# Kernel tuning notes

Hardware: AMD Instinct MI355X
Metric: run time of the kernel (lower is better)

## Reference

```python
import jax, jax.numpy as jnp
import numpy as np

H = 200  # hidden size
I = 129  # input features (n_fft bins)


def _lstm_layer(x, w_ih, w_hh, b_ih, b_hh):
    """PyTorch-convention LSTM. x: [B,T,I]; w_ih: [4H,I]; w_hh: [4H,H].
    Gate order i, f, g, o. Returns hidden sequence [B,T,H]."""
    B, T, _ = x.shape
    Hh = w_hh.shape[1]
    # Precompute input contribution for all timesteps (one big GEMM).
    xg = jnp.einsum('bti,gi->btg', x, w_ih) + b_ih + b_hh  # [B,T,4H]
    xg = jnp.swapaxes(xg, 0, 1)  # [T,B,4H] time-major for scan

    def step(carry, xg_t):
        h, c = carry
        g = xg_t + h @ w_hh.T  # [B,4H]
        i, f, gg, o = jnp.split(g, 4, axis=-1)
        i = jax.nn.sigmoid(i)
        f = jax.nn.sigmoid(f)
        gg = jnp.tanh(gg)
        o = jax.nn.sigmoid(o)
        c = f * c + i * gg
        h = o * jnp.tanh(c)
        return (h, c), h

    h0 = jnp.zeros((B, Hh), x.dtype)
    (_, _), hs = jax.lax.scan(step, (h0, h0), xg)
    return jnp.swapaxes(hs, 0, 1)  # [B,T,H]


def setup_inputs() -> dict:
    key = jax.random.key(0)
    ks = jax.random.split(key, 16)
    B, T = 256, 600
    s1 = 1.0 / np.sqrt(H)
    u = lambda k, shape: jax.random.uniform(k, shape, jnp.float32, -s1, s1)
    return {
        'x': jax.random.normal(ks[0], (B, I, T), jnp.float32),
        'w_ih1': u(ks[1], (4 * H, I)),
        'w_hh1': u(ks[2], (4 * H, H)),
        'b_ih1': u(ks[3], (4 * H,)),
        'b_hh1': u(ks[4], (4 * H,)),
        'w_ih2': u(ks[5], (4 * H, H)),
        'w_hh2': u(ks[6], (4 * H, H)),
        'b_ih2': u(ks[7], (4 * H,)),
        'b_hh2': u(ks[8], (4 * H,)),
        'fc1_w': u(ks[9], (I, H)),
        'fc1_b': u(ks[10], (I,)),
        'fc2_w': u(ks[11], (I, I)),
        'fc2_b': u(ks[12], (I,)),
    }


def reference(x, w_ih1, w_hh1, b_ih1, b_hh1,
              w_ih2, w_hh2, b_ih2, b_hh2,
              fc1_w, fc1_b, fc2_w, fc2_b):
    lstm_in = jnp.transpose(x, (0, 2, 1))  # [B,T,129]
    h1 = _lstm_layer(lstm_in, w_ih1, w_hh1, b_ih1, b_hh1)  # [B,T,200]
    h2 = _lstm_layer(h1, w_ih2, w_hh2, b_ih2, b_hh2)       # [B,T,200]
    y = jax.nn.relu(h2 @ fc1_w.T + fc1_b)                  # [B,T,129]
    y = jax.nn.sigmoid(y @ fc2_w.T + fc2_b)                # [B,T,129]
    return jnp.transpose(y, (0, 2, 1))                     # [B,129,T]
```

## Files before the change

### kernel.cpp

```cpp
#include <hip/hip_runtime.h>

typedef unsigned short u16;
typedef short short8 __attribute__((ext_vector_type(8)));
typedef float f32x4 __attribute__((ext_vector_type(4)));
typedef unsigned short u16x4 __attribute__((ext_vector_type(4)));

#define B_  256
#define T_  600
#define TC_ 75
#define HID 200
#define G4  800
#define HSTR 232

__device__ __forceinline__ float bf2f(u16 u) {
  union { unsigned int i; float f; } v; v.i = ((unsigned int)u) << 16; return v.f;
}
__device__ __forceinline__ u16 f2bf(float f) {
  union { float f; unsigned int i; } v; v.f = f;
  unsigned int r = v.i + 0x7FFFu + ((v.i >> 16) & 1u);
  return (u16)(r >> 16);
}
__device__ __forceinline__ float sigm(float x) {
  float e = __expf(-x);
  return __builtin_amdgcn_rcpf(1.f + e);
}

#define BARRIER_LGKM() asm volatile("s_waitcnt lgkmcnt(0)\n\ts_barrier" ::: "memory")
#define BARRIER_ONLY() asm volatile("s_barrier" ::: "memory")

__global__ __launch_bounds__(256) void padperm_k(const float* __restrict__ src,
                                                 u16* __restrict__ dst,
                                                 int rows, int srows, int scols,
                                                 int dcols, int perm) {
  int idx = blockIdx.x * 256 + threadIdx.x;
  if (idx >= rows * dcols) return;
  int r = idx / dcols, c = idx - r * dcols;
  int sr = perm ? ((r & 3) * 200 + (r >> 2)) : r;
  dst[idx] = (r < srows && c < scols) ? f2bf(src[(size_t)sr * scols + c]) : (u16)0;
}

__global__ __launch_bounds__(256) void transpose_k(const float* __restrict__ x,
                                                   u16* __restrict__ xTq, int t0) {
  __shared__ u16 tile[129 * 65];
  const int b = blockIdx.y;
  const int tt0 = blockIdx.x * 64;
  const int tid = threadIdx.x;
  for (int idx = tid; idx < 129 * 64; idx += 256) {
    int i = idx >> 6, tt = idx & 63;
    int t = t0 + tt0 + tt;
    tile[i * 65 + tt] = (tt0 + tt < TC_ && t < T_)
        ? f2bf(x[((size_t)b * 129 + i) * T_ + t]) : (u16)0;
  }
  __syncthreads();
  for (int idx = tid; idx < 64 * 160; idx += 256) {
    int tt = idx / 160, i = idx - tt * 160;
    if (tt0 + tt < TC_)
      xTq[((size_t)b * TC_ + tt0 + tt) * 160 + i] = (i < 129) ? tile[i * 65 + tt] : (u16)0;
  }
}

template<int ASRC, int LDK, int NSRC, int NSTORE, int BPERM, int ACT, int OUTM, int CHUNK>
__global__ __launch_bounds__(256, 2) void gemm_k(
    const u16* __restrict__ A, const u16* __restrict__ W,
    const float* __restrict__ B1, const float* __restrict__ B2,
    void* __restrict__ outv, int ldout, int t0) {
  constexpr int NCH = LDK / 8;
  constexpr int KT = LDK / 32;
  __shared__ u16 la[128 * LDK];
  __shared__ float lbias[128];
  const int tid = threadIdx.x;
  const int mb = blockIdx.x, nb = blockIdx.y;

  for (int idx = tid; idx < 128 * NCH; idx += 256) {
    int row = idx / NCH, c = idx - row * NCH;
    int m = mb * 128 + row;
    size_t arow;
    if (CHUNK) {
      int b = m / TC_;
      int tt = m - b * TC_;
      arow = (size_t)b * T_ + t0 + tt;
    } else {
      arow = (size_t)m;
    }
    short8 v = (short8)0;
    if (8 * c + 8 <= ASRC)
      v = *(const short8*)(A + arow * ASRC + 8 * c);
    *(short8*)(la + row * LDK + 8 * c) = v;
  }
  if (tid < 128) {
    int p = nb * 128 + tid;
    float bv = 0.f;
    if (p < NSRC) {
      int orig = BPERM ? ((p & 3) * 200 + (p >> 2)) : p;
      bv = B1[orig];
      if (BPERM) bv += B2[orig];
    }
    lbias[tid] = bv;
  }
  __syncthreads();

  const int w = tid >> 6, l = tid & 63;
  const int quad = l >> 4, l15 = l & 15;
  const int mq = (w >> 1) * 64, nq = (w & 1) * 64;

  const u16* wrow[4];
#pragma unroll
  for (int nt = 0; nt < 4; ++nt) {
    int p = nb * 128 + nq + nt * 16 + l15;
    wrow[nt] = W + (size_t)((p < NSRC) ? p : 0) * LDK;
  }

  f32x4 acc[4][4];
#pragma unroll
  for (int i = 0; i < 4; ++i)
#pragma unroll
    for (int j = 0; j < 4; ++j) acc[i][j] = (f32x4)0.f;

#pragma unroll
  for (int kt = 0; kt < KT; ++kt) {
    const int k0 = kt * 32 + quad * 8;
    short8 bf[4];
#pragma unroll
    for (int nt = 0; nt < 4; ++nt) bf[nt] = *(const short8*)(wrow[nt] + k0);
    short8 af[4];
#pragma unroll
    for (int mt = 0; mt < 4; ++mt)
      af[mt] = *(const short8*)(la + (mq + mt * 16 + l15) * LDK + k0);
#pragma unroll
    for (int mt = 0; mt < 4; ++mt)
#pragma unroll
      for (int nt = 0; nt < 4; ++nt)
        acc[mt][nt] = __builtin_amdgcn_mfma_f32_16x16x32_bf16(af[mt], bf[nt],
                                                              acc[mt][nt], 0, 0, 0);
  }

#pragma unroll
  for (int mt = 0; mt < 4; ++mt) {
#pragma unroll
    for (int nt = 0; nt < 4; ++nt) {
#pragma unroll
      for (int r = 0; r < 4; ++r) {
        int rowl = mq + mt * 16 + quad * 4 + r;
        int coln = nq + nt * 16 + l15;
        int pg = nb * 128 + coln;
        if (pg < NSTORE) {
          float v = (pg < NSRC) ? (acc[mt][nt][r] + lbias[coln]) : 0.f;
          if (ACT == 1) v = fmaxf(v, 0.f);
          if (ACT == 2) v = sigm(v);
          size_t m = (size_t)mb * 128 + rowl;
          if (OUTM == 0) {
            ((u16*)outv)[m * (size_t)ldout + pg] = f2bf(v);
          } else {
            int b = (int)(m / T_);
            int t = (int)(m - (size_t)b * T_);
            ((float*)outv)[((size_t)b * 129 + pg) * T_ + t] = v;
          }
        }
      }
    }
  }
}

__device__ __forceinline__ void rec_body(const u16* __restrict__ xgq,
                                         const u16* __restrict__ whh,
                                         u16* __restrict__ hout,
                                         float* __restrict__ cst,
                                         int t0, int blk) {
  __shared__ u16 hbuf[16 * HSTR];
  __shared__ u16 w45[50 * 2 * 512];
  __shared__ u16 w6lds[50 * 128];

  const int tid = threadIdx.x;
  const int w = tid >> 6, l = tid & 63;
  const int quad = l >> 4, l15 = l & 15;
  const int b0 = blk * 16;
  const int nslots = (w < 2) ? 4 : 3;

  short8 wreg[4][4];
#pragma unroll
  for (int s = 0; s < 4; ++s) {
    int tile = w + 16 * s;
    int p = tile * 16 + l15;
    int orig = (p & 3) * 200 + (p >> 2);
    const char* wbase = (const char*)whh + (size_t)orig * 400;
#pragma unroll
    for (int kk = 0; kk < 4; ++kk) {
      short8 v = (short8)0;
      if (s < nslots)
        v = *(const short8*)(wbase + kk * 64 + quad * 16);
      wreg[s][kk] = v;
    }
    if (s < nslots) {
#pragma unroll
      for (int j = 0; j < 2; ++j) {
        short8 v = *(const short8*)(wbase + (4 + j) * 64 + quad * 16);
        *(short8*)(w45 + ((size_t)tile * 2 + j) * 512 + l15 * 32 + quad * 8) = v;
      }
      if (quad == 0) {
        short8 v6 = *(const short8*)(wbase + 384);
        *(short8*)(w6lds + tile * 128 + l15 * 8) = v6;
      }
    }
  }
  for (int i = tid; i < 16 * HSTR; i += 1024) hbuf[i] = 0;

  float c[4];
  u16 hreg[4];
#pragma unroll
  for (int s = 0; s < 4; ++s) { c[s] = 0.f; hreg[s] = 0; }
  if (t0 != 0) {
#pragma unroll
    for (int s = 0; s < 4; ++s)
      if (s < nslots) {
        int unit = (w + 16 * s) * 4 + quad;
        hreg[s] = hout[((size_t)(b0 + l15) * T_ + (t0 - 1)) * HID + unit];
        c[s] = cst[(size_t)(b0 + l15) * HID + unit];
      }
  }

  const u16* xptr = xgq + (size_t)(b0 + l15) * TC_ * G4 + w * 16 + quad * 4;
  u16x4 xv[4];
#pragma unroll
  for (int s = 0; s < 4; ++s)
    xv[s] = (s < nslots) ? *(const u16x4*)(xptr + s * 256) : (u16x4)0;

  u16* hptr = hout + ((size_t)(b0 + l15) * T_ + t0) * HID;

  __syncthreads();

  for (int t = 0; t < TC_; ++t) {
#pragma unroll
    for (int s = 0; s < 4; ++s)
      if (s < nslots)
        hbuf[l15 * HSTR + (w + 16 * s) * 4 + quad] = hreg[s];
    BARRIER_LGKM();

    if (t > 0) {
#pragma unroll
      for (int s = 0; s < 4; ++s)
        if (s < nslots)
          hptr[(size_t)(t - 1) * HID + (w + 16 * s) * 4 + quad] = hreg[s];
    }

    f32x4 acc[4];
#pragma unroll
    for (int s = 0; s < 4; ++s) acc[s] = (f32x4)0.f;
#pragma unroll
    for (int kk = 0; kk < 4; ++kk) {
      short8 hf = *(const short8*)(hbuf + l15 * HSTR + kk * 32 + quad * 8);
#pragma unroll
      for (int s = 0; s < 4; ++s)
        if (s < nslots)
          acc[s] = __builtin_amdgcn_mfma_f32_16x16x32_bf16(wreg[s][kk], hf, acc[s], 0, 0, 0);
    }
#pragma unroll
    for (int j = 0; j < 2; ++j) {
      short8 hf = *(const short8*)(hbuf + l15 * HSTR + (4 + j) * 32 + quad * 8);
#pragma unroll
      for (int s = 0; s < 4; ++s)
        if (s < nslots) {
          short8 wz = *(const short8*)(w45 + ((size_t)(w + 16 * s) * 2 + j) * 512
                                       + l15 * 32 + quad * 8);
          acc[s] = __builtin_amdgcn_mfma_f32_16x16x32_bf16(wz, hf, acc[s], 0, 0, 0);
        }
    }
    {
      short8 hf = *(const short8*)(hbuf + l15 * HSTR + 192 + quad * 8);
#pragma unroll
      for (int s = 0; s < 4; ++s)
        if (s < nslots) {
          short8 wz = (short8)0;
          if (quad == 0)
            wz = *(const short8*)(w6lds + (w + 16 * s) * 128 + l15 * 8);
          acc[s] = __builtin_amdgcn_mfma_f32_16x16x32_bf16(wz, hf, acc[s], 0, 0, 0);
        }
    }

#pragma unroll
    for (int s = 0; s < 4; ++s) {
      if (s < nslots) {
        float vi = acc[s][0] + bf2f(xv[s][0]);
        float vf = acc[s][1] + bf2f(xv[s][1]);
        float vg = acc[s][2] + bf2f(xv[s][2]);
        float vo = acc[s][3] + bf2f(xv[s][3]);
        float iv = sigm(vi);
        float fv = sigm(vf);
        float gv = 2.f * sigm(2.f * vg) - 1.f;
        float ov = sigm(vo);
        float cn = fv * c[s] + iv * gv;
        c[s] = cn;
        float th = 2.f * sigm(2.f * cn) - 1.f;
        hreg[s] = f2bf(ov * th);
      }
    }

    if (t + 1 < TC_) {
      const u16* xp = xptr + (size_t)(t + 1) * G4;
#pragma unroll
      for (int s = 0; s < 4; ++s)
        if (s < nslots) xv[s] = *(const u16x4*)(xp + s * 256);
    }
    BARRIER_ONLY();
  }

#pragma unroll
  for (int s = 0; s < 4; ++s)
    if (s < nslots) {
      int unit = (w + 16 * s) * 4 + quad;
      hptr[(size_t)(TC_ - 1) * HID + unit] = hreg[s];
      cst[(size_t)(b0 + l15) * HID + unit] = c[s];
    }
}

__global__ __launch_bounds__(1024) void recp_k(
    const u16* __restrict__ xgA, const u16* __restrict__ whhA,
    u16* __restrict__ hA, float* __restrict__ cstA, int t0A,
    const u16* __restrict__ xgB, const u16* __restrict__ whhB,
    u16* __restrict__ hB, float* __restrict__ cstB, int t0B, int nA) {
  const int bb = blockIdx.x;
  const u16* xg; const u16* whh; u16* ho; float* cs; int t0, blk;
  if (bb < nA) { xg = xgA; whh = whhA; ho = hA; cs = cstA; t0 = t0A; blk = bb; }
  else         { xg = xgB; whh = whhB; ho = hB; cs = cstB; t0 = t0B; blk = bb - nA; }
  rec_body(xg, whh, ho, cs, t0, blk);
}

extern "C" void kernel_launch(void* const* d_in, const int* in_sizes, int n_in,
                              void* d_out, int out_size, void* d_ws, size_t ws_size,
                              hipStream_t stream) {
  (void)in_sizes; (void)n_in; (void)out_size; (void)ws_size;
  const float* x     = (const float*)d_in[0];
  const float* w_ih1 = (const float*)d_in[1];
  const float* w_hh1 = (const float*)d_in[2];
  const float* b_ih1 = (const float*)d_in[3];
  const float* b_hh1 = (const float*)d_in[4];
  const float* w_ih2 = (const float*)d_in[5];
  const float* w_hh2 = (const float*)d_in[6];
  const float* b_ih2 = (const float*)d_in[7];
  const float* b_hh2 = (const float*)d_in[8];
  const float* fc1_w = (const float*)d_in[9];
  const float* fc1_b = (const float*)d_in[10];
  const float* fc2_w = (const float*)d_in[11];
  const float* fc2_b = (const float*)d_in[12];
  float* out = (float*)d_out;

  char* ws = (char*)d_ws;
  u16*   xgA   = (u16*)(ws);
  u16*   xgB   = (u16*)(ws + 30720000LL);
  u16*   h1    = (u16*)(ws + 61440000LL);
  u16*   h2    = (u16*)(ws + 122880000LL);
  u16*   xTq   = (u16*)(ws + 184320000LL);
  float* cst1  = (float*)(ws + 190464000LL);
  float* cst2  = (float*)(ws + 190668800LL);
  u16*   wp1   = (u16*)(ws + 190873600LL);
  u16*   wp2   = (u16*)(ws + 191129600LL);
  u16*   fc1p  = (u16*)(ws + 191488000LL);
  u16*   fc2p  = (u16*)(ws + 191545792LL);
  u16*   whh1c = (u16*)(ws + 191587072LL);
  u16*   whh2c = (u16*)(ws + 191907072LL);
  u16*   y1    = h1;

  padperm_k<<<(800 * 160 + 255) / 256, 256, 0, stream>>>(w_ih1, wp1, 800, 800, 129, 160, 1);
  padperm_k<<<(800 * 224 + 255) / 256, 256, 0, stream>>>(w_ih2, wp2, 800, 800, 200, 224, 1);
  padperm_k<<<(129 * 224 + 255) / 256, 256, 0, stream>>>(fc1_w, fc1p, 129, 129, 200, 224, 0);
  padperm_k<<<(129 * 160 + 255) / 256, 256, 0, stream>>>(fc2_w, fc2p, 129, 129, 129, 160, 0);
  padperm_k<<<(800 * 200 + 255) / 256, 256, 0, stream>>>(w_hh1, whh1c, 800, 800, 200, 200, 0);
  padperm_k<<<(800 * 200 + 255) / 256, 256, 0, stream>>>(w_hh2, whh2c, 800, 800, 200, 200, 0);

  transpose_k<<<dim3(2, 256), 256, 0, stream>>>(x, xTq, 0);
  gemm_k<160, 160, 800, 800, 1, 0, 0, 0>
      <<<dim3(150, 7), 256, 0, stream>>>(xTq, wp1, b_ih1, b_hh1, xgA, 800, 0);
  recp_k<<<dim3(16), 1024, 0, stream>>>(xgA, whh1c, h1, cst1, 0,
                                        xgA, whh1c, h1, cst1, 0, 16);

  for (int i = 0; i < 7; ++i) {
    const int tA = (i + 1) * TC_;
    const int tB = i * TC_;
    transpose_k<<<dim3(2, 256), 256, 0, stream>>>(x, xTq, tA);
    gemm_k<160, 160, 800, 800, 1, 0, 0, 0>
        <<<dim3(150, 7), 256, 0, stream>>>(xTq, wp1, b_ih1, b_hh1, xgA, 800, 0);
    gemm_k<200, 224, 800, 800, 1, 0, 0, 1>
        <<<dim3(150, 7), 256, 0, stream>>>(h1, wp2, b_ih2, b_hh2, xgB, 800, tB);
    recp_k<<<dim3(32), 1024, 0, stream>>>(xgA, whh1c, h1, cst1, tA,
                                          xgB, whh2c, h2, cst2, tB, 16);
  }

  gemm_k<200, 224, 800, 800, 1, 0, 0, 1>
      <<<dim3(150, 7), 256, 0, stream>>>(h1, wp2, b_ih2, b_hh2, xgB, 800, 7 * TC_);
  recp_k<<<dim3(16), 1024, 0, stream>>>(xgA, whh1c, h1, cst1, 0,
                                        xgB, whh2c, h2, cst2, 7 * TC_, 0);

  gemm_k<200, 224, 129, 144, 0, 1, 0, 0>
      <<<dim3(1200, 2), 256, 0, stream>>>(h2, fc1p, fc1_b, fc1_b, y1, 144, 0);
  gemm_k<144, 160, 129, 129, 0, 2, 1, 0>
      <<<dim3(1200, 2), 256, 0, stream>>>(y1, fc2p, fc2_b, fc2_b, out, 0, 0);
}
```

Before: 2.759 ms.

## Double-buffer recurrent hidden-state LDS to use one barrier per timestep

Replaces the single hidden-state LDS buffer with a ping-pong pair so each step reads h from one buffer and writes the new h into the other, removing one of the two per-step barriers in the recurrent loop. The global h store now happens right after computing rather than at the start of the next step. It also specializes the per-wave slot count into explicit three-plus-optional-fourth code paths, packs the LDS into one 16-byte-aligned shared array, and pins the waves-per-EU attribute to steer register allocation. The cost is a larger LDS footprint for the second h buffer.

```diff
diff --git a/kernel.cpp b/kernel.cpp
--- a/kernel.cpp
+++ b/kernel.cpp
@@ -26,7 +26,6 @@
 }
 
 #define BARRIER_LGKM() asm volatile("s_waitcnt lgkmcnt(0)\n\ts_barrier" ::: "memory")
-#define BARRIER_ONLY() asm volatile("s_barrier" ::: "memory")
 
 __global__ __launch_bounds__(256) void padperm_k(const float* __restrict__ src,
                                                  u16* __restrict__ dst,
@@ -165,163 +164,174 @@
                                          const u16* __restrict__ whh,
                                          u16* __restrict__ hout,
                                          float* __restrict__ cst,
-                                         int t0, int blk) {
-  __shared__ u16 hbuf[16 * HSTR];
-  __shared__ u16 w45[50 * 2 * 512];
-  __shared__ u16 w6lds[50 * 128];
+                                         int t0, int blk, char* smem) {
+  u16* hb  = (u16*)smem;
+  u16* w45 = (u16*)(smem + 14848);
+  u16* w6  = (u16*)(smem + 117248);
 
   const int tid = threadIdx.x;
   const int w = tid >> 6, l = tid & 63;
   const int quad = l >> 4, l15 = l & 15;
   const int b0 = blk * 16;
-  const int nslots = (w < 2) ? 4 : 3;
+  const bool four = (w < 2);
 
   short8 wreg[4][4];
 #pragma unroll
   for (int s = 0; s < 4; ++s) {
+    const bool act = (s < 3) || four;
     int tile = w + 16 * s;
     int p = tile * 16 + l15;
     int orig = (p & 3) * 200 + (p >> 2);
-    const char* wbase = (const char*)whh + (size_t)orig * 400;
-#pragma unroll
-    for (int kk = 0; kk < 4; ++kk) {
-      short8 v = (short8)0;
-      if (s < nslots)
-        v = *(const short8*)(wbase + kk * 64 + quad * 16);
-      wreg[s][kk] = v;
-    }
-    if (s < nslots) {
-#pragma unroll
-      for (int j = 0; j < 2; ++j) {
-        short8 v = *(const short8*)(wbase + (4 + j) * 64 + quad * 16);
-        *(short8*)(w45 + ((size_t)tile * 2 + j) * 512 + l15 * 32 + quad * 8) = v;
-      }
-      if (quad == 0) {
-        short8 v6 = *(const short8*)(wbase + 384);
-        *(short8*)(w6lds + tile * 128 + l15 * 8) = v6;
-      }
-    }
-  }
-  for (int i = tid; i < 16 * HSTR; i += 1024) hbuf[i] = 0;
-
-  float c[4];
-  u16 hreg[4];
+    const u16* wb = whh + (size_t)orig * HID;
+#pragma unroll
+    for (int kk = 0; kk < 4; ++kk)
+      wreg[s][kk] = act ? *(const short8*)(wb + kk * 32 + quad * 8) : (short8)0;
+    if (act) {
+#pragma unroll
+      for (int j = 0; j < 2; ++j)
+        *(short8*)(w45 + (tile * 2 + j) * 512 + l * 8) =
+            *(const short8*)(wb + (4 + j) * 32 + quad * 8);
+      if (quad == 0)
+        *(short8*)(w6 + tile * 128 + l15 * 8) = *(const short8*)(wb + 192);
+    }
+  }
+  { int bsel = tid >> 9, r = (tid >> 5) & 15, cc = tid & 31;
+    hb[bsel * (16 * HSTR) + r * HSTR + 200 + cc] = 0; }
+
+  float c[4]; u16 hreg[4];
 #pragma unroll
   for (int s = 0; s < 4; ++s) { c[s] = 0.f; hreg[s] = 0; }
+  float* cstp = cst + (size_t)(b0 + l15) * HID;
   if (t0 != 0) {
 #pragma unroll
-    for (int s = 0; s < 4; ++s)
-      if (s < nslots) {
-        int unit = (w + 16 * s) * 4 + quad;
-        hreg[s] = hout[((size_t)(b0 + l15) * T_ + (t0 - 1)) * HID + unit];
-        c[s] = cst[(size_t)(b0 + l15) * HID + unit];
-      }
+    for (int s = 0; s < 3; ++s) {
+      int unit = (w + 16 * s) * 4 + quad;
+      hreg[s] = hout[((size_t)(b0 + l15) * T_ + (t0 - 1)) * HID + unit];
+      c[s] = cstp[unit];
+    }
+    if (four) {
+      int unit = (w + 48) * 4 + quad;
+      hreg[3] = hout[((size_t)(b0 + l15) * T_ + (t0 - 1)) * HID + unit];
+      c[3] = cstp[unit];
+    }
   }
 
   const u16* xptr = xgq + (size_t)(b0 + l15) * TC_ * G4 + w * 16 + quad * 4;
   u16x4 xv[4];
 #pragma unroll
-  for (int s = 0; s < 4; ++s)
-    xv[s] = (s < nslots) ? *(const u16x4*)(xptr + s * 256) : (u16x4)0;
+  for (int s = 0; s < 3; ++s) xv[s] = *(const u16x4*)(xptr + s * 256);
+  xv[3] = four ? *(const u16x4*)(xptr + 768) : (u16x4)0;
 
   u16* hptr = hout + ((size_t)(b0 + l15) * T_ + t0) * HID;
 
+#pragma unroll
+  for (int s = 0; s < 3; ++s)
+    hb[l15 * HSTR + (w + 16 * s) * 4 + quad] = hreg[s];
+  if (four)
+    hb[l15 * HSTR + (w + 48) * 4 + quad] = hreg[3];
+
   __syncthreads();
 
   for (int t = 0; t < TC_; ++t) {
-#pragma unroll
-    for (int s = 0; s < 4; ++s)
-      if (s < nslots)
-        hbuf[l15 * HSTR + (w + 16 * s) * 4 + quad] = hreg[s];
-    BARRIER_LGKM();
-
-    if (t > 0) {
-#pragma unroll
-      for (int s = 0; s < 4; ++s)
-        if (s < nslots)
-          hptr[(size_t)(t - 1) * HID + (w + 16 * s) * 4 + quad] = hreg[s];
-    }
+    const u16* hr = hb + (t & 1) * (16 * HSTR);
+    u16* hw = hb + ((t + 1) & 1) * (16 * HSTR);
 
     f32x4 acc[4];
 #pragma unroll
     for (int s = 0; s < 4; ++s) acc[s] = (f32x4)0.f;
+
 #pragma unroll
     for (int kk = 0; kk < 4; ++kk) {
-      short8 hf = *(const short8*)(hbuf + l15 * HSTR + kk * 32 + quad * 8);
-#pragma unroll
-      for (int s = 0; s < 4; ++s)
-        if (s < nslots)
-          acc[s] = __builtin_amdgcn_mfma_f32_16x16x32_bf16(wreg[s][kk], hf, acc[s], 0, 0, 0);
+      short8 hf = *(const short8*)(hr + l15 * HSTR + kk * 32 + quad * 8);
+      acc[0] = __builtin_amdgcn_mfma_f32_16x16x32_bf16(wreg[0][kk], hf, acc[0], 0, 0, 0);
+      acc[1] = __builtin_amdgcn_mfma_f32_16x16x32_bf16(wreg[1][kk], hf, acc[1], 0, 0, 0);
+      acc[2] = __builtin_amdgcn_mfma_f32_16x16x32_bf16(wreg[2][kk], hf, acc[2], 0, 0, 0);
+      if (four)
+        acc[3] = __builtin_amdgcn_mfma_f32_16x16x32_bf16(wreg[3][kk], hf, acc[3], 0, 0, 0);
     }
 #pragma unroll
     for (int j = 0; j < 2; ++j) {
-      short8 hf = *(const short8*)(hbuf + l15 * HSTR + (4 + j) * 32 + quad * 8);
-#pragma unroll
-      for (int s = 0; s < 4; ++s)
-        if (s < nslots) {
-          short8 wz = *(const short8*)(w45 + ((size_t)(w + 16 * s) * 2 + j) * 512
-                                       + l15 * 32 + quad * 8);
-          acc[s] = __builtin_amdgcn_mfma_f32_16x16x32_bf16(wz, hf, acc[s], 0, 0, 0);
-        }
+      short8 hf = *(const short8*)(hr + l15 * HSTR + (4 + j) * 32 + quad * 8);
+#pragma unroll
+      for (int s = 0; s < 3; ++s) {
+        short8 wz = *(const short8*)(w45 + ((w + 16 * s) * 2 + j) * 512 + l * 8);
+        acc[s] = __builtin_amdgcn_mfma_f32_16x16x32_bf16(wz, hf, acc[s], 0, 0, 0);
+      }
+      if (four) {
+        short8 wz = *(const short8*)(w45 + ((w + 48) * 2 + j) * 512 + l * 8);
+        acc[3] = __builtin_amdgcn_mfma_f32_16x16x32_bf16(wz, hf, acc[3], 0, 0, 0);
+      }
     }
     {
-      short8 hf = *(const short8*)(hbuf + l15 * HSTR + 192 + quad * 8);
-#pragma unroll
-      for (int s = 0; s < 4; ++s)
-        if (s < nslots) {
-          short8 wz = (short8)0;
-          if (quad == 0)
-            wz = *(const short8*)(w6lds + (w + 16 * s) * 128 + l15 * 8);
-          acc[s] = __builtin_amdgcn_mfma_f32_16x16x32_bf16(wz, hf, acc[s], 0, 0, 0);
-        }
+      short8 hf = *(const short8*)(hr + l15 * HSTR + 192 + quad * 8);
+#pragma unroll
+      for (int s = 0; s < 3; ++s) {
+        short8 wz = (short8)0;
+        if (quad == 0)
+          wz = *(const short8*)(w6 + (w + 16 * s) * 128 + l15 * 8);
+        acc[s] = __builtin_amdgcn_mfma_f32_16x16x32_bf16(wz, hf, acc[s], 0, 0, 0);
+      }
+      if (four) {
+        short8 wz = (short8)0;
+        if (quad == 0)
+          wz = *(const short8*)(w6 + (w + 48) * 128 + l15 * 8);
+        acc[3] = __builtin_amdgcn_mfma_f32_16x16x32_bf16(wz, hf, acc[3], 0, 0, 0);
+      }
     }
 
 #pragma unroll
     for (int s = 0; s < 4; ++s) {
-      if (s < nslots) {
-        float vi = acc[s][0] + bf2f(xv[s][0]);
-        float vf = acc[s][1] + bf2f(xv[s][1]);
-        float vg = acc[s][2] + bf2f(xv[s][2]);
-        float vo = acc[s][3] + bf2f(xv[s][3]);
-        float iv = sigm(vi);
-        float fv = sigm(vf);
-        float gv = 2.f * sigm(2.f * vg) - 1.f;
-        float ov = sigm(vo);
-        float cn = fv * c[s] + iv * gv;
-        c[s] = cn;
-        float th = 2.f * sigm(2.f * cn) - 1.f;
-        hreg[s] = f2bf(ov * th);
-      }
-    }
+      if (s == 3 && !four) break;
+      float vi = acc[s][0] + bf2f(xv[s][0]);
+      float vf = acc[s][1] + bf2f(xv[s][1]);
+      float vg = acc[s][2] + bf2f(xv[s][2]);
+      float vo = acc[s][3] + bf2f(xv[s][3]);
+      float iv = sigm(vi);
+      float fv = sigm(vf);
+      float gv = 2.f * sigm(2.f * vg) - 1.f;
+      float ov = sigm(vo);
+      float cn = fv * c[s] + iv * gv;
+      c[s] = cn;
+      float th = 2.f * sigm(2.f * cn) - 1.f;
+      hreg[s] = f2bf(ov * th);
+    }
+
+#pragma unroll
+    for (int s = 0; s < 3; ++s)
+      hw[l15 * HSTR + (w + 16 * s) * 4 + quad] = hreg[s];
+    if (four)
+      hw[l15 * HSTR + (w + 48) * 4 + quad] = hreg[3];
+
+#pragma unroll
+    for (int s = 0; s < 3; ++s)
+      hptr[(size_t)t * HID + (w + 16 * s) * 4 + quad] = hreg[s];
+    if (four)
+      hptr[(size_t)t * HID + (w + 48) * 4 + quad] = hreg[3];
 
     if (t + 1 < TC_) {
       const u16* xp = xptr + (size_t)(t + 1) * G4;
 #pragma unroll
-      for (int s = 0; s < 4; ++s)
-        if (s < nslots) xv[s] = *(const u16x4*)(xp + s * 256);
-    }
-    BARRIER_ONLY();
-  }
-
-#pragma unroll
-  for (int s = 0; s < 4; ++s)
-    if (s < nslots) {
-      int unit = (w + 16 * s) * 4 + quad;
-      hptr[(size_t)(TC_ - 1) * HID + unit] = hreg[s];
-      cst[(size_t)(b0 + l15) * HID + unit] = c[s];
-    }
-}
-
-__global__ __launch_bounds__(1024) void recp_k(
-    const u16* __restrict__ xgA, const u16* __restrict__ whhA,
-    u16* __restrict__ hA, float* __restrict__ cstA, int t0A,
-    const u16* __restrict__ xgB, const u16* __restrict__ whhB,
-    u16* __restrict__ hB, float* __restrict__ cstB, int t0B, int nA) {
+      for (int s = 0; s < 3; ++s) xv[s] = *(const u16x4*)(xp + s * 256);
+      if (four) xv[3] = *(const u16x4*)(xp + 768);
+    }
+    BARRIER_LGKM();
+  }
+
+#pragma unroll
+  for (int s = 0; s < 3; ++s) cstp[(w + 16 * s) * 4 + quad] = c[s];
+  if (four) cstp[(w + 48) * 4 + quad] = c[3];
+}
+
+__global__ __attribute__((amdgpu_flat_work_group_size(1024, 1024),
+                          amdgpu_waves_per_eu(4, 4)))
+void recp_k(const u16* __restrict__ xgA, const u16* __restrict__ whhA,
+            u16* __restrict__ hA, float* __restrict__ cstA, int t0A,
+            const u16* __restrict__ xgB, const u16* __restrict__ whhB,
+            u16* __restrict__ hB, float* __restrict__ cstB, int t0B, int nA) {
+  __shared__ __align__(16) char smem[130048];
   const int bb = blockIdx.x;
-  const u16* xg; const u16* whh; u16* ho; float* cs; int t0, blk;
-  if (bb < nA) { xg = xgA; whh = whhA; ho = hA; cs = cstA; t0 = t0A; blk = bb; }
-  else         { xg = xgB; whh = whhB; ho = hB; cs = cstB; t0 = t0B; blk = bb - nA; }
-  rec_body(xg, whh, ho, cs, t0, blk);
+  if (bb < nA) rec_body(xgA, whhA, hA, cstA, t0A, bb, smem);
+  else         rec_body(xgB, whhB, hB, cstB, t0B, bb - nA, smem);
 }
 
 extern "C" void kernel_launch(void* const* d_in, const int* in_sizes, int n_in,
```

Measured after the change: 3.195 ms. 15.8% more time.
